# Optimization experiments

Hardware: AMD Instinct MI355X
Metric: run time of the kernel (lower is better)

The kernel has to match this reference:

```python
import jax, jax.numpy as jnp
import numpy as np

ALPHA = 0.2  # LeakyReLU negative slope
NEG = -9e15


def gat_layer(h, adj, W, a):
    # Faithful to the torch GAT: e_ij = leakyrelu(a^T [Wh_i || Wh_j])
    # = leakyrelu(a_src . Wh_i + a_dst . Wh_j); avoids the NxNx2F materialization.
    Wh = h @ W                              # [N, F]
    Fo = W.shape[1]
    a_src, a_dst = a[:Fo, 0], a[Fo:, 0]
    e = jax.nn.leaky_relu(
        (Wh @ a_src)[:, None] + (Wh @ a_dst)[None, :], negative_slope=ALPHA
    )                                        # [N, N]
    e = jnp.where(adj > 0, e, NEG)
    att = jax.nn.softmax(e, axis=1)          # dropout p=0 (eval)
    return jax.nn.elu(att @ Wh)


def gru_cell(x, h, W_ih, W_hh, b_ih, b_hh):
    # PyTorch GRUCell semantics.
    gi = x @ W_ih.T + b_ih                   # [N, 3F]
    gh = h @ W_hh.T + b_hh
    i_r, i_z, i_n = jnp.split(gi, 3, axis=1)
    h_r, h_z, h_n = jnp.split(gh, 3, axis=1)
    r = jax.nn.sigmoid(i_r + h_r)
    z = jax.nn.sigmoid(i_z + h_z)
    n = jnp.tanh(i_n + r * h_n)
    return (1.0 - z) * n + z * h


def setup_inputs() -> dict:
    key = jax.random.key(0)
    ks = jax.random.split(key, 10)
    N, nfeat, nhid, nout = 8192, 256, 128, 128
    x = jax.random.normal(ks[0], (N, nfeat), dtype=jnp.float32)
    # sparse random binary adjacency (~32 avg degree) + self loops
    adj = (jax.random.uniform(ks[1], (N, N)) < 0.004).astype(jnp.float32)
    adj = jnp.maximum(adj, jnp.eye(N, dtype=jnp.float32))
    h_prev = jnp.zeros((N, nout), dtype=jnp.float32)

    def xavier(k, shape, gain=1.414):
        fan_in, fan_out = shape[0], shape[1]
        b = gain * np.sqrt(6.0 / (fan_in + fan_out))
        return jax.random.uniform(k, shape, jnp.float32, -b, b)

    W1 = xavier(ks[2], (nfeat, nhid))
    a1 = xavier(ks[3], (2 * nhid, 1))
    W2 = xavier(ks[4], (nhid, nout))
    a2 = xavier(ks[5], (2 * nout, 1))
    s = 1.0 / np.sqrt(nout)
    W_ih = jax.random.uniform(ks[6], (3 * nout, nout), jnp.float32, -s, s)
    W_hh = jax.random.uniform(ks[7], (3 * nout, nout), jnp.float32, -s, s)
    b_ih = jax.random.uniform(ks[8], (3 * nout,), jnp.float32, -s, s)
    b_hh = jax.random.uniform(ks[9], (3 * nout,), jnp.float32, -s, s)
    return {"x": x, "adj": adj, "h_prev": h_prev, "W1": W1, "a1": a1,
            "W2": W2, "a2": a2, "W_ih": W_ih, "W_hh": W_hh,
            "b_ih": b_ih, "b_hh": b_hh}


def reference(x, adj, h_prev, W1, a1, W2, a2, W_ih, W_hh, b_ih, b_hh):
    x1 = gat_layer(x, adj, W1, a1)
    h_spat = gat_layer(x1, adj, W2, a2)
    return gru_cell(h_spat, h_prev, W_ih, W_hh, b_ih, b_hh)
```

## Files before the change

kernel.cpp:

```cpp
#include <hip/hip_runtime.h>
#include <math.h>

#define N_NODES 8192
#define CAP 128
#define LRELU_ALPHA 0.2f

__global__ void build_adj_kernel(const float* __restrict__ adj, int* __restrict__ idx,
                                 int* __restrict__ counts) {
  __shared__ int cnt;
  int i = blockIdx.x;
  int t = threadIdx.x;
  int lane = t & 63;
  if (t == 0) cnt = 0;
  __syncthreads();
  const float4* row = (const float4*)(adj + (size_t)i * N_NODES);
  int* outp = idx + (size_t)i * CAP;
  for (int b = t; b < N_NODES / 4; b += 256) {
    float4 v = row[b];
    int j0 = b * 4;
#pragma unroll
    for (int c = 0; c < 4; c++) {
      float x = (c == 0) ? v.x : (c == 1) ? v.y : (c == 2) ? v.z : v.w;
      bool hit = x > 0.f;
      unsigned long long mask = __ballot(hit);
      if (mask) {
        int base = 0;
        if (lane == 0) base = atomicAdd(&cnt, __popcll(mask));
        base = __shfl(base, 0);
        if (hit) {
          int pos = base + __popcll(mask & ((1ull << lane) - 1ull));
          if (pos < CAP) outp[pos] = j0 + c;
        }
      }
    }
  }
  __syncthreads();
  if (t == 0) counts[i] = cnt > CAP ? CAP : cnt;
}

template <int K>
__global__ void gemm_srcdst(const float* __restrict__ A, const float* __restrict__ W,
                            const float* __restrict__ a, float* __restrict__ Wh,
                            float* __restrict__ src, float* __restrict__ dst) {
  __shared__ float As[16][K];
  __shared__ float sp[16][128];
  __shared__ float dp[16][128];
  int t = threadIdx.x;
  int c = t & 127;
  int half = t >> 7;
  int r0 = blockIdx.x * 16;
  const float4* Ab4 = (const float4*)(A + (size_t)r0 * K);
  float4* As4 = (float4*)(&As[0][0]);
  for (int l = t; l < 16 * K / 4; l += 256) As4[l] = Ab4[l];
  __syncthreads();
  float acc[8] = {0.f, 0.f, 0.f, 0.f, 0.f, 0.f, 0.f, 0.f};
  const float* Asl = &As[half * 8][0];
#pragma unroll 4
  for (int k = 0; k < K; k++) {
    float wv = W[k * 128 + c];
#pragma unroll
    for (int r = 0; r < 8; r++) acc[r] += Asl[r * K + k] * wv;
  }
  float as = a[c], ad = a[128 + c];
#pragma unroll
  for (int r = 0; r < 8; r++) {
    int row = half * 8 + r;
    Wh[(size_t)(r0 + row) * 128 + c] = acc[r];
    sp[row][c] = acc[r] * as;
    dp[row][c] = acc[r] * ad;
  }
  __syncthreads();
  int row = t >> 4, l16 = t & 15;
  float s = 0.f, d = 0.f;
#pragma unroll
  for (int m = 0; m < 8; m++) {
    s += sp[row][l16 + 16 * m];
    d += dp[row][l16 + 16 * m];
  }
#pragma unroll
  for (int off = 8; off > 0; off >>= 1) {
    s += __shfl_down(s, off, 16);
    d += __shfl_down(d, off, 16);
  }
  if (l16 == 0) {
    src[r0 + row] = s;
    dst[r0 + row] = d;
  }
}

__global__ void gat_aggregate_kernel(const float* __restrict__ Wh, const float* __restrict__ src,
                                     const float* __restrict__ dst, const int* __restrict__ idx,
                                     const int* __restrict__ counts, float* __restrict__ outp) {
  __shared__ float w[CAP];
  __shared__ int jn[CAP];
  __shared__ float redm[2];
  __shared__ float reds[2];
  int i = blockIdx.x, t = threadIdx.x;
  int cnt = counts[i];
  float si = src[i];
  float v = -1e30f;
  if (t < cnt) {
    int j = idx[(size_t)i * CAP + t];
    jn[t] = j;
    float e = si + dst[j];
    v = e > 0.f ? e : LRELU_ALPHA * e;
  }
  float m = v;
#pragma unroll
  for (int off = 32; off > 0; off >>= 1) m = fmaxf(m, __shfl_xor(m, off));
  if ((t & 63) == 0) redm[t >> 6] = m;
  __syncthreads();
  float M = fmaxf(redm[0], redm[1]);
  float ex = 0.f;
  if (t < cnt) {
    ex = expf(v - M);
    w[t] = ex;
  }
  float s = ex;
#pragma unroll
  for (int off = 32; off > 0; off >>= 1) s += __shfl_xor(s, off);
  if ((t & 63) == 0) reds[t >> 6] = s;
  __syncthreads();
  float inv = 1.f / (reds[0] + reds[1]);
  float acc = 0.f;
  int k = 0;
  for (; k + 4 <= cnt; k += 4) {
    float w0 = w[k], w1 = w[k + 1], w2 = w[k + 2], w3 = w[k + 3];
    int j0 = jn[k], j1 = jn[k + 1], j2 = jn[k + 2], j3 = jn[k + 3];
    acc += w0 * Wh[(size_t)j0 * 128 + t] + w1 * Wh[(size_t)j1 * 128 + t] +
           w2 * Wh[(size_t)j2 * 128 + t] + w3 * Wh[(size_t)j3 * 128 + t];
  }
  for (; k < cnt; k++) acc += w[k] * Wh[(size_t)jn[k] * 128 + t];
  acc *= inv;
  outp[(size_t)i * 128 + t] = acc > 0.f ? acc : expf(acc) - 1.f;
}

__global__ void transpose2_kernel(const float* __restrict__ Wi, const float* __restrict__ Whm,
                                  float* __restrict__ WiT, float* __restrict__ WhT) {
  int n = blockIdx.x * blockDim.x + threadIdx.x;
  if (n < 384 * 128) {
    int r = n >> 7;
    int c = n & 127;
    WiT[c * 384 + r] = Wi[n];
    WhT[c * 384 + r] = Whm[n];
  }
}

__global__ void gru_kernel(const float* __restrict__ x, const float* __restrict__ h,
                           const float* __restrict__ WiT, const float* __restrict__ WhT,
                           const float* __restrict__ b_ih, const float* __restrict__ b_hh,
                           float* __restrict__ outp) {
  __shared__ float xs[16][128];
  __shared__ float hs[16][128];
  int t = threadIdx.x;
  int c = t & 127;
  int half = t >> 7;
  int r0 = blockIdx.x * 16;
  {
    const float4* xb = (const float4*)(x + (size_t)r0 * 128);
    const float4* hb = (const float4*)(h + (size_t)r0 * 128);
    float4* xs4 = (float4*)(&xs[0][0]);
    float4* hs4 = (float4*)(&hs[0][0]);
    for (int l = t; l < 16 * 128 / 4; l += 256) {
      xs4[l] = xb[l];
      hs4[l] = hb[l];
    }
  }
  __syncthreads();
  const float* xsl = &xs[half * 8][0];
  const float* hsl = &hs[half * 8][0];
  float rg[8], zg[8];
  {
    float ai[8] = {0.f}, ah[8] = {0.f};
#pragma unroll 4
    for (int k = 0; k < 128; k++) {
      float wi = WiT[k * 384 + c];
      float wh = WhT[k * 384 + c];
#pragma unroll
      for (int r = 0; r < 8; r++) {
        ai[r] += xsl[r * 128 + k] * wi;
        ah[r] += hsl[r * 128 + k] * wh;
      }
    }
    float bi = b_ih[c], bh = b_hh[c];
#pragma unroll
    for (int r = 0; r < 8; r++) rg[r] = 1.f / (1.f + expf(-(ai[r] + bi + ah[r] + bh)));
  }
  {
    float ai[8] = {0.f}, ah[8] = {0.f};
#pragma unroll 4
    for (int k = 0; k < 128; k++) {
      float wi = WiT[k * 384 + 128 + c];
      float wh = WhT[k * 384 + 128 + c];
#pragma unroll
      for (int r = 0; r < 8; r++) {
        ai[r] += xsl[r * 128 + k] * wi;
        ah[r] += hsl[r * 128 + k] * wh;
      }
    }
    float bi = b_ih[128 + c], bh = b_hh[128 + c];
#pragma unroll
    for (int r = 0; r < 8; r++) zg[r] = 1.f / (1.f + expf(-(ai[r] + bi + ah[r] + bh)));
  }
  {
    float ai[8] = {0.f}, ah[8] = {0.f};
#pragma unroll 4
    for (int k = 0; k < 128; k++) {
      float wi = WiT[k * 384 + 256 + c];
      float wh = WhT[k * 384 + 256 + c];
#pragma unroll
      for (int r = 0; r < 8; r++) {
        ai[r] += xsl[r * 128 + k] * wi;
        ah[r] += hsl[r * 128 + k] * wh;
      }
    }
    float bi = b_ih[256 + c], bh = b_hh[256 + c];
#pragma unroll
    for (int r = 0; r < 8; r++) {
      float n = tanhf(ai[r] + bi + rg[r] * (ah[r] + bh));
      float o = (1.f - zg[r]) * n + zg[r] * hsl[r * 128 + c];
      outp[(size_t)(r0 + half * 8 + r) * 128 + c] = o;
    }
  }
}

extern "C" void kernel_launch(void* const* d_in, const int* in_sizes, int n_in,
                              void* d_out, int out_size, void* d_ws, size_t ws_size,
                              hipStream_t stream) {
  const float* x     = (const float*)d_in[0];
  const float* adj   = (const float*)d_in[1];
  const float* hprev = (const float*)d_in[2];
  const float* W1    = (const float*)d_in[3];
  const float* a1    = (const float*)d_in[4];
  const float* W2    = (const float*)d_in[5];
  const float* a2    = (const float*)d_in[6];
  const float* W_ih  = (const float*)d_in[7];
  const float* W_hh  = (const float*)d_in[8];
  const float* b_ih  = (const float*)d_in[9];
  const float* b_hh  = (const float*)d_in[10];
  float* outp = (float*)d_out;

  char* p = (char*)d_ws;
  float* Wh1    = (float*)p; p += (size_t)N_NODES * 128 * 4;
  float* Wh2    = (float*)p; p += (size_t)N_NODES * 128 * 4;
  float* x1     = (float*)p; p += (size_t)N_NODES * 128 * 4;
  float* h_spat = (float*)p; p += (size_t)N_NODES * 128 * 4;
  float* src1   = (float*)p; p += (size_t)N_NODES * 4;
  float* dst1   = (float*)p; p += (size_t)N_NODES * 4;
  float* src2   = (float*)p; p += (size_t)N_NODES * 4;
  float* dst2   = (float*)p; p += (size_t)N_NODES * 4;
  float* WiT    = (float*)p; p += (size_t)384 * 128 * 4;
  float* WhT    = (float*)p; p += (size_t)384 * 128 * 4;
  int*   counts = (int*)p;   p += (size_t)N_NODES * 4;
  int*   idxbuf = (int*)p;   p += (size_t)N_NODES * CAP * 4;

  build_adj_kernel<<<N_NODES, 256, 0, stream>>>(adj, idxbuf, counts);
  transpose2_kernel<<<(384 * 128 + 255) / 256, 256, 0, stream>>>(W_ih, W_hh, WiT, WhT);

  gemm_srcdst<256><<<N_NODES / 16, 256, 0, stream>>>(x, W1, a1, Wh1, src1, dst1);
  gat_aggregate_kernel<<<N_NODES, 128, 0, stream>>>(Wh1, src1, dst1, idxbuf, counts, x1);

  gemm_srcdst<128><<<N_NODES / 16, 256, 0, stream>>>(x1, W2, a2, Wh2, src2, dst2);
  gat_aggregate_kernel<<<N_NODES, 128, 0, stream>>>(Wh2, src2, dst2, idxbuf, counts, h_spat);

  gru_kernel<<<N_NODES / 16, 256, 0, stream>>>(h_spat, hprev, WiT, WhT, b_ih, b_hh, outp);
}
```

Measured before the change: 532.8 us.

## Fuse adjacency build, first GEMM and weight transpose into one heterogeneous launch

Merges the adjacency compaction, the first Wh/src/dst GEMM and the GRU weight transpose into a single kernel whose blocks are split by role. The goal is to let the small GEMM and transpose work overlap the bandwidth-bound 256MB adjacency scan and to save launches. The adjacency scan now uses nontemporal vector loads and a per-thread atomic instead of a ballot per element. The GEMM and GRU kernels use 8-row tiles for more blocks and replace the shared-memory src/dst reduction with wave shuffles. Neighbor order within a row becomes nondeterministic, which can change float summation order.

```diff
diff --git a/kernel.cpp b/kernel.cpp
--- a/kernel.cpp
+++ b/kernel.cpp
@@ -5,87 +5,102 @@
 #define CAP 128
 #define LRELU_ALPHA 0.2f
 
-__global__ void build_adj_kernel(const float* __restrict__ adj, int* __restrict__ idx,
-                                 int* __restrict__ counts) {
-  __shared__ int cnt;
-  int i = blockIdx.x;
-  int t = threadIdx.x;
-  int lane = t & 63;
-  if (t == 0) cnt = 0;
-  __syncthreads();
-  const float4* row = (const float4*)(adj + (size_t)i * N_NODES);
-  int* outp = idx + (size_t)i * CAP;
-  for (int b = t; b < N_NODES / 4; b += 256) {
-    float4 v = row[b];
-    int j0 = b * 4;
-#pragma unroll
-    for (int c = 0; c < 4; c++) {
-      float x = (c == 0) ? v.x : (c == 1) ? v.y : (c == 2) ? v.z : v.w;
-      bool hit = x > 0.f;
-      unsigned long long mask = __ballot(hit);
-      if (mask) {
-        int base = 0;
-        if (lane == 0) base = atomicAdd(&cnt, __popcll(mask));
-        base = __shfl(base, 0);
-        if (hit) {
-          int pos = base + __popcll(mask & ((1ull << lane) - 1ull));
-          if (pos < CAP) outp[pos] = j0 + c;
-        }
-      }
-    }
-  }
-  __syncthreads();
-  if (t == 0) counts[i] = cnt > CAP ? CAP : cnt;
-}
+typedef float v4f __attribute__((ext_vector_type(4)));
 
 template <int K>
-__global__ void gemm_srcdst(const float* __restrict__ A, const float* __restrict__ W,
-                            const float* __restrict__ a, float* __restrict__ Wh,
-                            float* __restrict__ src, float* __restrict__ dst) {
-  __shared__ float As[16][K];
-  __shared__ float sp[16][128];
-  __shared__ float dp[16][128];
-  int t = threadIdx.x;
-  int c = t & 127;
-  int half = t >> 7;
-  int r0 = blockIdx.x * 16;
+__device__ __forceinline__ void gemm_srcdst_body(
+    int r0, int t, const float* __restrict__ A, const float* __restrict__ W,
+    const float* __restrict__ a, float* __restrict__ Wh, float* __restrict__ src,
+    float* __restrict__ dst, float* As, float (*red)[4][2]) {
+  int c = t & 127, half = t >> 7;
   const float4* Ab4 = (const float4*)(A + (size_t)r0 * K);
-  float4* As4 = (float4*)(&As[0][0]);
-  for (int l = t; l < 16 * K / 4; l += 256) As4[l] = Ab4[l];
-  __syncthreads();
-  float acc[8] = {0.f, 0.f, 0.f, 0.f, 0.f, 0.f, 0.f, 0.f};
-  const float* Asl = &As[half * 8][0];
+  float4* As4 = (float4*)As;
+#pragma unroll
+  for (int l = t; l < 8 * K / 4; l += 256) As4[l] = Ab4[l];
+  __syncthreads();
+  float acc[4] = {0.f, 0.f, 0.f, 0.f};
+  const float* Asl = As + (half * 4) * K;
 #pragma unroll 4
   for (int k = 0; k < K; k++) {
     float wv = W[k * 128 + c];
 #pragma unroll
-    for (int r = 0; r < 8; r++) acc[r] += Asl[r * K + k] * wv;
+    for (int r = 0; r < 4; r++) acc[r] += Asl[r * K + k] * wv;
   }
   float as = a[c], ad = a[128 + c];
-#pragma unroll
-  for (int r = 0; r < 8; r++) {
-    int row = half * 8 + r;
+  int wv_id = t >> 6, lane = t & 63;
+#pragma unroll
+  for (int r = 0; r < 4; r++) {
+    int row = half * 4 + r;
     Wh[(size_t)(r0 + row) * 128 + c] = acc[r];
-    sp[row][c] = acc[r] * as;
-    dp[row][c] = acc[r] * ad;
-  }
-  __syncthreads();
-  int row = t >> 4, l16 = t & 15;
-  float s = 0.f, d = 0.f;
-#pragma unroll
-  for (int m = 0; m < 8; m++) {
-    s += sp[row][l16 + 16 * m];
-    d += dp[row][l16 + 16 * m];
-  }
-#pragma unroll
-  for (int off = 8; off > 0; off >>= 1) {
-    s += __shfl_down(s, off, 16);
-    d += __shfl_down(d, off, 16);
-  }
-  if (l16 == 0) {
-    src[r0 + row] = s;
-    dst[r0 + row] = d;
-  }
+    float s = acc[r] * as, d = acc[r] * ad;
+#pragma unroll
+    for (int off = 32; off; off >>= 1) {
+      s += __shfl_xor(s, off);
+      d += __shfl_xor(d, off);
+    }
+    if (lane == 0) { red[wv_id][r][0] = s; red[wv_id][r][1] = d; }
+  }
+  __syncthreads();
+  if (t < 8) {
+    int wa = (t < 4) ? 0 : 2, rr = t & 3;
+    src[r0 + t] = red[wa][rr][0] + red[wa + 1][rr][0];
+    dst[r0 + t] = red[wa][rr][1] + red[wa + 1][rr][1];
+  }
+}
+
+#define ADJ_B 8192
+#define G1_B 1024
+#define TR_B 64
+__global__ void phase1_kernel(const float* __restrict__ adj, int* __restrict__ idx,
+                              int* __restrict__ counts, const float* __restrict__ x,
+                              const float* __restrict__ W1, const float* __restrict__ a1,
+                              float* __restrict__ Wh1, float* __restrict__ src1,
+                              float* __restrict__ dst1, const float* __restrict__ Wi,
+                              const float* __restrict__ Whm, float* __restrict__ WiT,
+                              float* __restrict__ WhT) {
+  __shared__ float As[8 * 256];
+  __shared__ float red[4][4][2];
+  __shared__ int cnt;
+  int t = threadIdx.x;
+  int bid = blockIdx.x;
+  if (bid < ADJ_B) {
+    if (t == 0) cnt = 0;
+    __syncthreads();
+    const v4f* row = (const v4f*)(adj + (size_t)bid * N_NODES);
+    int* outp = idx + (size_t)bid * CAP;
+#pragma unroll 2
+    for (int b = t; b < N_NODES / 4; b += 256) {
+      v4f v = __builtin_nontemporal_load(row + b);
+      int n = (v.x > 0.f) + (v.y > 0.f) + (v.z > 0.f) + (v.w > 0.f);
+      if (n) {
+        int p = atomicAdd(&cnt, n);
+        int j0 = b * 4;
+        if (v.x > 0.f) { if (p < CAP) outp[p] = j0;     p++; }
+        if (v.y > 0.f) { if (p < CAP) outp[p] = j0 + 1; p++; }
+        if (v.z > 0.f) { if (p < CAP) outp[p] = j0 + 2; p++; }
+        if (v.w > 0.f) { if (p < CAP) outp[p] = j0 + 3; p++; }
+      }
+    }
+    __syncthreads();
+    if (t == 0) counts[bid] = cnt > CAP ? CAP : cnt;
+  } else if (bid < ADJ_B + G1_B) {
+    gemm_srcdst_body<256>((bid - ADJ_B) * 8, t, x, W1, a1, Wh1, src1, dst1, As, red);
+  } else {
+    int gid = (bid - ADJ_B - G1_B) * 256 + t;
+    for (int n = gid; n < 384 * 128; n += TR_B * 256) {
+      int r = n >> 7, c = n & 127;
+      WiT[c * 384 + r] = Wi[n];
+      WhT[c * 384 + r] = Whm[n];
+    }
+  }
+}
+
+__global__ void gemm_srcdst2_kernel(const float* __restrict__ A, const float* __restrict__ W,
+                                    const float* __restrict__ a, float* __restrict__ Wh,
+                                    float* __restrict__ src, float* __restrict__ dst) {
+  __shared__ float As[8 * 128];
+  __shared__ float red[4][4][2];
+  gemm_srcdst_body<128>(blockIdx.x * 8, threadIdx.x, A, W, a, Wh, src, dst, As, red);
 }
 
 __global__ void gat_aggregate_kernel(const float* __restrict__ Wh, const float* __restrict__ src,
@@ -135,91 +150,74 @@
   outp[(size_t)i * 128 + t] = acc > 0.f ? acc : expf(acc) - 1.f;
 }
 
-__global__ void transpose2_kernel(const float* __restrict__ Wi, const float* __restrict__ Whm,
-                                  float* __restrict__ WiT, float* __restrict__ WhT) {
-  int n = blockIdx.x * blockDim.x + threadIdx.x;
-  if (n < 384 * 128) {
-    int r = n >> 7;
-    int c = n & 127;
-    WiT[c * 384 + r] = Wi[n];
-    WhT[c * 384 + r] = Whm[n];
-  }
-}
-
 __global__ void gru_kernel(const float* __restrict__ x, const float* __restrict__ h,
                            const float* __restrict__ WiT, const float* __restrict__ WhT,
                            const float* __restrict__ b_ih, const float* __restrict__ b_hh,
                            float* __restrict__ outp) {
-  __shared__ float xs[16][128];
-  __shared__ float hs[16][128];
-  int t = threadIdx.x;
-  int c = t & 127;
-  int half = t >> 7;
-  int r0 = blockIdx.x * 16;
+  __shared__ float xs[8 * 128];
+  __shared__ float hs[8 * 128];
+  int t = threadIdx.x, c = t & 127, half = t >> 7;
+  int r0 = blockIdx.x * 8;
   {
     const float4* xb = (const float4*)(x + (size_t)r0 * 128);
     const float4* hb = (const float4*)(h + (size_t)r0 * 128);
-    float4* xs4 = (float4*)(&xs[0][0]);
-    float4* hs4 = (float4*)(&hs[0][0]);
-    for (int l = t; l < 16 * 128 / 4; l += 256) {
-      xs4[l] = xb[l];
-      hs4[l] = hb[l];
-    }
-  }
-  __syncthreads();
-  const float* xsl = &xs[half * 8][0];
-  const float* hsl = &hs[half * 8][0];
-  float rg[8], zg[8];
-  {
-    float ai[8] = {0.f}, ah[8] = {0.f};
+    ((float4*)xs)[t] = xb[t];
+    ((float4*)hs)[t] = hb[t];
+  }
+  __syncthreads();
+  const float* xsl = xs + half * 4 * 128;
+  const float* hsl = hs + half * 4 * 128;
+  float rg[4], zg[4];
+  {
+    float ai[4] = {0.f}, ah[4] = {0.f};
 #pragma unroll 4
     for (int k = 0; k < 128; k++) {
       float wi = WiT[k * 384 + c];
       float wh = WhT[k * 384 + c];
 #pragma unroll
-      for (int r = 0; r < 8; r++) {
+      for (int r = 0; r < 4; r++) {
         ai[r] += xsl[r * 128 + k] * wi;
         ah[r] += hsl[r * 128 + k] * wh;
       }
     }
     float bi = b_ih[c], bh = b_hh[c];
 #pragma unroll
-    for (int r = 0; r < 8; r++) rg[r] = 1.f / (1.f + expf(-(ai[r] + bi + ah[r] + bh)));
-  }
-  {
-    float ai[8] = {0.f}, ah[8] = {0.f};
+    for (int r = 0; r < 4; r++) rg[r] = 1.f / (1.f + expf(-(ai[r] + bi + ah[r] + bh)));
+  }
+  {
+    float ai[4] = {0.f}, ah[4] = {0.f};
 #pragma unroll 4
     for (int k = 0; k < 128; k++) {
       float wi = WiT[k * 384 + 128 + c];
       float wh = WhT[k * 384 + 128 + c];
 #pragma unroll
-      for (int r = 0; r < 8; r++) {
+      for (int r = 0; r < 4; r++) {
         ai[r] += xsl[r * 128 + k] * wi;
         ah[r] += hsl[r * 128 + k] * wh;
       }
     }
     float bi = b_ih[128 + c], bh = b_hh[128 + c];
 #pragma unroll
-    for (int r = 0; r < 8; r++) zg[r] = 1.f / (1.f + expf(-(ai[r] + bi + ah[r] + bh)));
-  }
-  {
-    float ai[8] = {0.f}, ah[8] = {0.f};
+    for (int r = 0; r < 4; r++) zg[r] = 1.f / (1.f + expf(-(ai[r] + bi + ah[r] + bh)));
+  }
+  {
+    float ai[4] = {0.f}, ah[4] = {0.f};
 #pragma unroll 4
     for (int k = 0; k < 128; k++) {
       float wi = WiT[k * 384 + 256 + c];
       float wh = WhT[k * 384 + 256 + c];
 #pragma unroll
-      for (int r = 0; r < 8; r++) {
+      for (int r = 0; r < 4; r++) {
         ai[r] += xsl[r * 128 + k] * wi;
         ah[r] += hsl[r * 128 + k] * wh;
       }
     }
     float bi = b_ih[256 + c], bh = b_hh[256 + c];
 #pragma unroll
-    for (int r = 0; r < 8; r++) {
+    for (int r = 0; r < 4; r++) {
       float n = tanhf(ai[r] + bi + rg[r] * (ah[r] + bh));
       float o = (1.f - zg[r]) * n + zg[r] * hsl[r * 128 + c];
-      outp[(size_t)(r0 + half * 8 + r) * 128 + c] = o;
+      outp[(size_t)(r0 + half * 4 + r) * 128 + c] = o;
     }
   }
 }
@@ -254,14 +252,10 @@
   int*   counts = (int*)p;   p += (size_t)N_NODES * 4;
   int*   idxbuf = (int*)p;   p += (size_t)N_NODES * CAP * 4;
 
-  build_adj_kernel<<<N_NODES, 256, 0, stream>>>(adj, idxbuf, counts);
-  transpose2_kernel<<<(384 * 128 + 255) / 256, 256, 0, stream>>>(W_ih, W_hh, WiT, WhT);
-
-  gemm_srcdst<256><<<N_NODES / 16, 256, 0, stream>>>(x, W1, a1, Wh1, src1, dst1);
+  phase1_kernel<<<ADJ_B + G1_B + TR_B, 256, 0, stream>>>(
+      adj, idxbuf, counts, x, W1, a1, Wh1, src1, dst1, W_ih, W_hh, WiT, WhT);
   gat_aggregate_kernel<<<N_NODES, 128, 0, stream>>>(Wh1, src1, dst1, idxbuf, counts, x1);
-
-  gemm_srcdst<128><<<N_NODES / 16, 256, 0, stream>>>(x1, W2, a2, Wh2, src2, dst2);
+  gemm_srcdst2_kernel<<<N_NODES / 8, 256, 0, stream>>>(x1, W2, a2, Wh2, src2, dst2);
   gat_aggregate_kernel<<<N_NODES, 128, 0, stream>>>(Wh2, src2, dst2, idxbuf, counts, h_spat);
-
-  gru_kernel<<<N_NODES / 16, 256, 0, stream>>>(h_spat, hprev, WiT, WhT, b_ih, b_hh, outp);
-}
+  gru_kernel<<<N_NODES / 8, 256, 0, stream>>>(h_spat, hprev, WiT, WhT, b_ih, b_hh, outp);
+}
```

Result: faster. 490.6 us (-7.9%).
